# Performance work log

Measured on AMD Instinct MI355X. Metric: run time of the kernel, lower is better.

The kernel has to match this reference:

```python
import jax, jax.numpy as jnp
import numpy as np


def setup_inputs() -> dict:
    key = jax.random.key(0)
    k1, k2, k3, k4, k5 = jax.random.split(key, 5)
    B, T, H = 8, 2048, 1024
    s = 1.0 / np.sqrt(H)
    return {
        "x": jax.random.normal(k1, (B, T, H), dtype=jnp.float32),
        "W_ih": jax.random.normal(k2, (3 * H, H), dtype=jnp.float32) * s,
        "b_ih": jax.random.normal(k3, (3 * H,), dtype=jnp.float32) * s,
        "W_hh": jax.random.normal(k4, (3 * H, H), dtype=jnp.float32) * s,
        "b_hh": jax.random.normal(k5, (3 * H,), dtype=jnp.float32) * s,
    }


def reference(x, W_ih, b_ih, W_hh, b_hh):
    # x: [B, T, H]; W_ih/W_hh: [3H, H]; biases: [3H]
    B, T, H = x.shape
    # Precompute input-to-hidden projection in one batched matmul: [B, T, 3H]
    x_proj = jnp.einsum("bth,gh->btg", x, W_ih) + b_ih
    h0 = jnp.zeros((B, H), dtype=x.dtype)

    def step(h, g_x):
        # g_x: [B, 3H]
        g_h = h @ W_hh.T + b_hh  # [B, 3H]
        r = jax.nn.sigmoid(g_x[:, :H] + g_h[:, :H])
        z = jax.nn.sigmoid(g_x[:, H:2 * H] + g_h[:, H:2 * H])
        n = jnp.tanh(g_x[:, 2 * H:] + r * g_h[:, 2 * H:])
        h_new = (1 - z) * n + z * h
        return h_new, h_new

    # scan over time axis: move T to leading axis
    _, out = jax.lax.scan(step, h0, jnp.swapaxes(x_proj, 0, 1))  # out: [T, B, H]
    return jnp.swapaxes(out, 0, 1)  # [B, T, H]; dropout=0.0 (eval) is identity
```

## Files before the change

kernel.cpp:

```cpp
#include <hip/hip_runtime.h>

#define T_STEPS 2048
#define BATCH 8
#define HID 1024

#define XPROJ_F 50331648ull
#define HBUF64_BYTE_OFF 201326592ull

__device__ __forceinline__ float sigmoidf_(float x) {
    return 1.0f / (1.0f + __expf(-x));
}

__device__ __forceinline__ unsigned long long ld_u64_agent(const unsigned long long* p) {
    return __hip_atomic_load(p, __ATOMIC_RELAXED, __HIP_MEMORY_SCOPE_AGENT);
}
__device__ __forceinline__ void st_u64_agent(unsigned long long* p, unsigned long long v) {
    __hip_atomic_store(p, v, __ATOMIC_RELAXED, __HIP_MEMORY_SCOPE_AGENT);
}

__global__ __launch_bounds__(256) void gemm_xproj(
        const float* __restrict__ x, const float* __restrict__ Wih,
        const float* __restrict__ bih, float* __restrict__ xproj) {
    __shared__ float a_lds[16][128];
    __shared__ float b_lds[16][128];
    const int tid = threadIdx.x;
    const int m0 = blockIdx.x * 128;
    const int n0 = blockIdx.y * 128;
    const int tx = tid & 15, ty = tid >> 4;

    float acc[8][8];
#pragma unroll
    for (int i = 0; i < 8; i++)
#pragma unroll
        for (int jj = 0; jj < 8; jj++) acc[i][jj] = 0.f;

    for (int k0 = 0; k0 < 1024; k0 += 16) {
#pragma unroll
        for (int l = 0; l < 2; l++) {
            const int c = tid + l * 256;
            const int row = c >> 2;
            const int f4 = c & 3;
            float4 av = *reinterpret_cast<const float4*>(
                x + (size_t)(m0 + row) * 1024 + k0 + f4 * 4);
            float4 bv = *reinterpret_cast<const float4*>(
                Wih + (size_t)(n0 + row) * 1024 + k0 + f4 * 4);
            a_lds[f4 * 4 + 0][row] = av.x; a_lds[f4 * 4 + 1][row] = av.y;
            a_lds[f4 * 4 + 2][row] = av.z; a_lds[f4 * 4 + 3][row] = av.w;
            b_lds[f4 * 4 + 0][row] = bv.x; b_lds[f4 * 4 + 1][row] = bv.y;
            b_lds[f4 * 4 + 2][row] = bv.z; b_lds[f4 * 4 + 3][row] = bv.w;
        }
        __syncthreads();
#pragma unroll
        for (int kk = 0; kk < 16; kk++) {
            float a[8], b[8];
            *reinterpret_cast<float4*>(&a[0]) =
                *reinterpret_cast<float4*>(&a_lds[kk][ty * 8]);
            *reinterpret_cast<float4*>(&a[4]) =
                *reinterpret_cast<float4*>(&a_lds[kk][ty * 8 + 4]);
            *reinterpret_cast<float4*>(&b[0]) =
                *reinterpret_cast<float4*>(&b_lds[kk][tx * 8]);
            *reinterpret_cast<float4*>(&b[4]) =
                *reinterpret_cast<float4*>(&b_lds[kk][tx * 8 + 4]);
#pragma unroll
            for (int i = 0; i < 8; i++)
#pragma unroll
                for (int jj = 0; jj < 8; jj++)
                    acc[i][jj] = fmaf(a[i], b[jj], acc[i][jj]);
        }
        __syncthreads();
    }

    float bias[8];
    *reinterpret_cast<float4*>(&bias[0]) =
        *reinterpret_cast<const float4*>(bih + n0 + tx * 8);
    *reinterpret_cast<float4*>(&bias[4]) =
        *reinterpret_cast<const float4*>(bih + n0 + tx * 8 + 4);
    const int n_base = n0 + tx * 8;
    const int g = n_base >> 10;
    const int j0 = n_base & 1023;
#pragma unroll
    for (int i = 0; i < 8; i++) {
        const int m = m0 + ty * 8 + i;
        const int b = m >> 11;
        const int t = m & 2047;
        float* dst = xproj + (((size_t)t * 8 + b) * 3 + g) * 1024 + j0;
        float4 r0 = {acc[i][0] + bias[0], acc[i][1] + bias[1],
                     acc[i][2] + bias[2], acc[i][3] + bias[3]};
        float4 r1 = {acc[i][4] + bias[4], acc[i][5] + bias[5],
                     acc[i][6] + bias[6], acc[i][7] + bias[7]};
        *reinterpret_cast<float4*>(dst) = r0;
        *reinterpret_cast<float4*>(dst + 4) = r1;
    }
}

__global__ __launch_bounds__(256, 1) void gru_scan(
        const float* __restrict__ Whh, const float* __restrict__ bhh,
        const float* __restrict__ xproj, float* __restrict__ out,
        unsigned long long* __restrict__ hbuf64) {
    __shared__ float hshare[2][2 * HID];
    const int tid = threadIdx.x;
    const int bid = blockIdx.x;
    const int wave = tid >> 6;
    const int lane = tid & 63;
    const int group = bid >> 6;
    const int gb = bid & 63;
    const int b0 = group * 2;
    const int jbase = gb * 16 + wave * 4;

    float wf[3][4][16];
#pragma unroll
    for (int g = 0; g < 3; g++)
#pragma unroll
        for (int jj = 0; jj < 4; jj++)
#pragma unroll
            for (int i = 0; i < 16; i++)
                wf[g][jj][i] =
                    Whh[(size_t)(g * 1024 + jbase + jj) * 1024 + lane + 64 * i];

    const int jj_l = lane >> 1;
    const int bb_l = lane & 1;
    const int j_l = jbase + jj_l;
    const int b_l = b0 + bb_l;
    float bh0 = 0.f, bh1 = 0.f, bh2 = 0.f;
    if (lane < 8) {
        bh0 = bhh[j_l];
        bh1 = bhh[1024 + j_l];
        bh2 = bhh[2048 + j_l];
    }

    if (lane < 8) {
        const size_t xb = ((size_t)0 * 8 + b_l) * 3 * 1024 + j_l;
        const float gxr = xproj[xb];
        const float gxz = xproj[xb + 1024];
        const float gxn = xproj[xb + 2048];
        const float r = sigmoidf_(gxr + bh0);
        const float z = sigmoidf_(gxz + bh1);
        const float n = tanhf(gxn + r * bh2);
        const float hnew = (1.f - z) * n;
        st_u64_agent(hbuf64 + (size_t)b_l * HID + j_l,
                     ((unsigned long long)1u << 32) | __float_as_uint(hnew));
        out[(size_t)b_l * T_STEPS * HID + j_l] = hnew;
    }

    for (int t = 1; t < T_STEPS; t++) {
        float gxr = 0.f, gxz = 0.f, gxn = 0.f;
        if (lane < 8) {
            const size_t xb = ((size_t)t * 8 + b_l) * 3 * 1024 + j_l;
            gxr = xproj[xb];
            gxz = xproj[xb + 1024];
            gxn = xproj[xb + 2048];
        }

        const int par = (t - 1) & 1;
        const unsigned long long* src =
            hbuf64 + (size_t)par * 8192 + (size_t)b0 * HID;
        const unsigned expect = (unsigned)t;
        unsigned long long v[8];
#pragma unroll
        for (int i = 0; i < 8; i++)
            v[i] = ld_u64_agent(src + tid + 256 * i);
        for (;;) {
            unsigned bad = 0;
#pragma unroll
            for (int i = 0; i < 8; i++)
                bad |= (unsigned)(v[i] >> 32) ^ expect;
            if (bad == 0) break;
            __builtin_amdgcn_s_sleep(1);
#pragma unroll
            for (int i = 0; i < 8; i++)
                if ((unsigned)(v[i] >> 32) != expect)
                    v[i] = ld_u64_agent(src + tid + 256 * i);
        }
#pragma unroll
        for (int i = 0; i < 8; i++)
            hshare[par][tid + 256 * i] = __uint_as_float((unsigned)v[i]);
        __syncthreads();

        const float hprev = (lane < 8) ? hshare[par][bb_l * HID + j_l] : 0.f;

        float acc[3][8];
#pragma unroll
        for (int g = 0; g < 3; g++)
#pragma unroll
            for (int q = 0; q < 8; q++) acc[g][q] = 0.f;
#pragma unroll
        for (int bb = 0; bb < 2; bb++) {
            float hv[16];
#pragma unroll
            for (int i = 0; i < 16; i++)
                hv[i] = hshare[par][bb * HID + lane + 64 * i];
#pragma unroll
            for (int g = 0; g < 3; g++)
#pragma unroll
                for (int jj = 0; jj < 4; jj++)
#pragma unroll
                    for (int i = 0; i < 16; i++)
                        acc[g][jj * 2 + bb] =
                            fmaf(wf[g][jj][i], hv[i], acc[g][jj * 2 + bb]);
        }

        float a4[3][4];
#pragma unroll
        for (int g = 0; g < 3; g++)
#pragma unroll
            for (int k = 0; k < 4; k++) {
                const float e = acc[g][2 * k], o = acc[g][2 * k + 1];
                const float give = (lane & 1) ? e : o;
                const float keep = (lane & 1) ? o : e;
                a4[g][k] = keep + __shfl_xor(give, 1);
            }
        float a2[3][2];
#pragma unroll
        for (int g = 0; g < 3; g++)
#pragma unroll
            for (int k = 0; k < 2; k++) {
                const float e = a4[g][2 * k], o = a4[g][2 * k + 1];
                const float give = (lane & 2) ? e : o;
                const float keep = (lane & 2) ? o : e;
                a2[g][k] = keep + __shfl_xor(give, 2);
            }
        float a1[3];
#pragma unroll
        for (int g = 0; g < 3; g++) {
            const float e = a2[g][0], o = a2[g][1];
            const float give = (lane & 4) ? e : o;
            const float keep = (lane & 4) ? o : e;
            a1[g] = keep + __shfl_xor(give, 4);
        }
#pragma unroll
        for (int m = 8; m <= 32; m <<= 1)
#pragma unroll
            for (int g = 0; g < 3; g++) a1[g] += __shfl_xor(a1[g], m);

        if (lane < 8) {
            const float r = sigmoidf_(gxr + a1[0] + bh0);
            const float z = sigmoidf_(gxz + a1[1] + bh1);
            const float n = tanhf(gxn + r * (a1[2] + bh2));
            const float hnew = (1.f - z) * n + z * hprev;
            st_u64_agent(hbuf64 + (size_t)(t & 1) * 8192 + (size_t)b_l * HID + j_l,
                         ((unsigned long long)(unsigned)(t + 1) << 32) |
                             __float_as_uint(hnew));
            out[((size_t)b_l * T_STEPS + t) * HID + j_l] = hnew;
        }
    }
}

extern "C" void kernel_launch(void* const* d_in, const int* in_sizes, int n_in,
                              void* d_out, int out_size, void* d_ws,
                              size_t ws_size, hipStream_t stream) {
    const float* x    = (const float*)d_in[0];
    const float* Wih  = (const float*)d_in[1];
    const float* bih  = (const float*)d_in[2];
    const float* Whh  = (const float*)d_in[3];
    const float* bhh  = (const float*)d_in[4];
    float* outp = (float*)d_out;

    float* xproj = (float*)d_ws;
    unsigned long long* hbuf64 =
        (unsigned long long*)((char*)d_ws + HBUF64_BYTE_OFF);

    dim3 g1(128, 24);
    gemm_xproj<<<g1, 256, 0, stream>>>(x, Wih, bih, xproj);
    gru_scan<<<256, 256, 0, stream>>>(Whh, bhh, xproj, outp, hbuf64);
}
```

Measured before the change: 8.267 ms.

## Pack two hidden values per flag word and assign one batch per block

Each block now handles one batch row and 32 hidden units instead of two batch rows and 16, so it holds twice the W_hh slice in registers. Hidden-state exchange packs two floats into each 64-bit word and uses bit 30 of the low float as a parity tag instead of a full 32-bit step counter. Hidden values are clamped just below 1 so that bit is always free. This halves the polled global traffic per block and reduces spin-wait loads. The cost is more register pressure, with a risk of spills, and the xproj layout is switched to batch-major to match.

```diff
diff --git a/kernel.cpp b/kernel.cpp
--- a/kernel.cpp
+++ b/kernel.cpp
@@ -83,7 +83,7 @@
         const int m = m0 + ty * 8 + i;
         const int b = m >> 11;
         const int t = m & 2047;
-        float* dst = xproj + (((size_t)t * 8 + b) * 3 + g) * 1024 + j0;
+        float* dst = xproj + (((size_t)b * 2048 + t) * 3 + g) * 1024 + j0;
         float4 r0 = {acc[i][0] + bias[0], acc[i][1] + bias[1],
                      acc[i][2] + bias[2], acc[i][3] + bias[3]};
         float4 r1 = {acc[i][4] + bias[4], acc[i][5] + bias[5],
@@ -97,106 +97,102 @@
         const float* __restrict__ Whh, const float* __restrict__ bhh,
         const float* __restrict__ xproj, float* __restrict__ out,
         unsigned long long* __restrict__ hbuf64) {
-    __shared__ float hshare[2][2 * HID];
+    __shared__ float hshare[2][HID];
     const int tid = threadIdx.x;
     const int bid = blockIdx.x;
     const int wave = tid >> 6;
     const int lane = tid & 63;
-    const int group = bid >> 6;
-    const int gb = bid & 63;
-    const int b0 = group * 2;
-    const int jbase = gb * 16 + wave * 4;
-
-    float wf[3][4][16];
+    const int b = bid & 7;
+    const int gb = bid >> 3;
+    const int jb_w = gb * 32 + wave * 8;
+    const int jw = jb_w + (lane & 7);
+
+    float wf[3][8][16];
 #pragma unroll
     for (int g = 0; g < 3; g++)
 #pragma unroll
-        for (int jj = 0; jj < 4; jj++)
+        for (int jj = 0; jj < 8; jj++)
 #pragma unroll
             for (int i = 0; i < 16; i++)
                 wf[g][jj][i] =
-                    Whh[(size_t)(g * 1024 + jbase + jj) * 1024 + lane + 64 * i];
-
-    const int jj_l = lane >> 1;
-    const int bb_l = lane & 1;
-    const int j_l = jbase + jj_l;
-    const int b_l = b0 + bb_l;
-    float bh0 = 0.f, bh1 = 0.f, bh2 = 0.f;
-    if (lane < 8) {
-        bh0 = bhh[j_l];
-        bh1 = bhh[1024 + j_l];
-        bh2 = bhh[2048 + j_l];
-    }
-
-    if (lane < 8) {
-        const size_t xb = ((size_t)0 * 8 + b_l) * 3 * 1024 + j_l;
+                    Whh[(size_t)(g * 1024 + jb_w + jj) * 1024 + lane + 64 * i];
+
+    const float bh0 = bhh[jw];
+    const float bh1 = bhh[1024 + jw];
+    const float bh2 = bhh[2048 + jw];
+    const float CL = 0x1.fffffep-1f;
+
+    {
+        const size_t xb = ((size_t)b * 2048 + 0) * 3 * 1024 + jw;
         const float gxr = xproj[xb];
         const float gxz = xproj[xb + 1024];
         const float gxn = xproj[xb + 2048];
         const float r = sigmoidf_(gxr + bh0);
         const float z = sigmoidf_(gxz + bh1);
         const float n = tanhf(gxn + r * bh2);
-        const float hnew = (1.f - z) * n;
-        st_u64_agent(hbuf64 + (size_t)b_l * HID + j_l,
-                     ((unsigned long long)1u << 32) | __float_as_uint(hnew));
-        out[(size_t)b_l * T_STEPS * HID + j_l] = hnew;
+        float hnew = (1.f - z) * n;
+        hnew = fminf(fmaxf(hnew, -CL), CL);
+        const float hodd = __shfl_xor(hnew, 1);
+        const unsigned lo = __float_as_uint(hnew) | (1u << 30);
+        const unsigned hi = __float_as_uint(hodd);
+        if (lane < 8) {
+            if ((lane & 1) == 0)
+                st_u64_agent(hbuf64 + (size_t)b * 512 + ((jb_w + lane) >> 1),
+                             ((unsigned long long)hi << 32) | lo);
+            out[((size_t)b * 2048 + 0) * 1024 + jw] = hnew;
+        }
     }
 
     for (int t = 1; t < T_STEPS; t++) {
-        float gxr = 0.f, gxz = 0.f, gxn = 0.f;
-        if (lane < 8) {
-            const size_t xb = ((size_t)t * 8 + b_l) * 3 * 1024 + j_l;
-            gxr = xproj[xb];
-            gxz = xproj[xb + 1024];
-            gxn = xproj[xb + 2048];
-        }
+        const size_t xb = ((size_t)b * 2048 + t) * 3 * 1024 + jw;
+        const float gxr = xproj[xb];
+        const float gxz = xproj[xb + 1024];
+        const float gxn = xproj[xb + 2048];
 
         const int par = (t - 1) & 1;
         const unsigned long long* src =
-            hbuf64 + (size_t)par * 8192 + (size_t)b0 * HID;
-        const unsigned expect = (unsigned)t;
-        unsigned long long v[8];
-#pragma unroll
-        for (int i = 0; i < 8; i++)
-            v[i] = ld_u64_agent(src + tid + 256 * i);
+            hbuf64 + (size_t)par * 4096 + (size_t)b * 512;
+        const unsigned expect = (((unsigned)(t - 1) >> 1) & 1u) ^ 1u;
+        unsigned long long v0 = ld_u64_agent(src + tid);
+        unsigned long long v1 = ld_u64_agent(src + tid + 256);
         for (;;) {
-            unsigned bad = 0;
-#pragma unroll
-            for (int i = 0; i < 8; i++)
-                bad |= (unsigned)(v[i] >> 32) ^ expect;
-            if (bad == 0) break;
+            const unsigned t0 = ((unsigned)(v0 >> 30)) & 1u;
+            const unsigned t1 = ((unsigned)(v1 >> 30)) & 1u;
+            if (((t0 ^ expect) | (t1 ^ expect)) == 0u) break;
             __builtin_amdgcn_s_sleep(1);
-#pragma unroll
-            for (int i = 0; i < 8; i++)
-                if ((unsigned)(v[i] >> 32) != expect)
-                    v[i] = ld_u64_agent(src + tid + 256 * i);
-        }
-#pragma unroll
-        for (int i = 0; i < 8; i++)
-            hshare[par][tid + 256 * i] = __uint_as_float((unsigned)v[i]);
+            if (t0 != expect) v0 = ld_u64_agent(src + tid);
+            if (t1 != expect) v1 = ld_u64_agent(src + tid + 256);
+        }
+        {
+            float2 p0, p1;
+            p0.x = __uint_as_float((unsigned)v0 & 0xBFFFFFFFu);
+            p0.y = __uint_as_float((unsigned)(v0 >> 32));
+            p1.x = __uint_as_float((unsigned)v1 & 0xBFFFFFFFu);
+            p1.y = __uint_as_float((unsigned)(v1 >> 32));
+            *reinterpret_cast<float2*>(&hshare[par][2 * tid]) = p0;
+            *reinterpret_cast<float2*>(&hshare[par][2 * tid + 512]) = p1;
+        }
         __syncthreads();
 
-        const float hprev = (lane < 8) ? hshare[par][bb_l * HID + j_l] : 0.f;
+        const float hprev = hshare[par][jw];
 
         float acc[3][8];
 #pragma unroll
         for (int g = 0; g < 3; g++)
 #pragma unroll
             for (int q = 0; q < 8; q++) acc[g][q] = 0.f;
-#pragma unroll
-        for (int bb = 0; bb < 2; bb++) {
+        {
             float hv[16];
 #pragma unroll
             for (int i = 0; i < 16; i++)
-                hv[i] = hshare[par][bb * HID + lane + 64 * i];
+                hv[i] = hshare[par][lane + 64 * i];
 #pragma unroll
             for (int g = 0; g < 3; g++)
 #pragma unroll
-                for (int jj = 0; jj < 4; jj++)
+                for (int jj = 0; jj < 8; jj++)
 #pragma unroll
                     for (int i = 0; i < 16; i++)
-                        acc[g][jj * 2 + bb] =
-                            fmaf(wf[g][jj][i], hv[i], acc[g][jj * 2 + bb]);
+                        acc[g][jj] = fmaf(wf[g][jj][i], hv[i], acc[g][jj]);
         }
 
         float a4[3][4];
@@ -232,15 +228,21 @@
 #pragma unroll
             for (int g = 0; g < 3; g++) a1[g] += __shfl_xor(a1[g], m);
 
+        const float r = sigmoidf_(gxr + a1[0] + bh0);
+        const float z = sigmoidf_(gxz + a1[1] + bh1);
+        const float n = tanhf(gxn + r * (a1[2] + bh2));
+        float hnew = (1.f - z) * n + z * hprev;
+        hnew = fminf(fmaxf(hnew, -CL), CL);
+        const float hodd = __shfl_xor(hnew, 1);
+        const unsigned tagst = (((unsigned)t >> 1) & 1u) ^ 1u;
+        const unsigned lo = __float_as_uint(hnew) | (tagst << 30);
+        const unsigned hi = __float_as_uint(hodd);
         if (lane < 8) {
-            const float r = sigmoidf_(gxr + a1[0] + bh0);
-            const float z = sigmoidf_(gxz + a1[1] + bh1);
-            const float n = tanhf(gxn + r * (a1[2] + bh2));
-            const float hnew = (1.f - z) * n + z * hprev;
-            st_u64_agent(hbuf64 + (size_t)(t & 1) * 8192 + (size_t)b_l * HID + j_l,
-                         ((unsigned long long)(unsigned)(t + 1) << 32) |
-                             __float_as_uint(hnew));
-            out[((size_t)b_l * T_STEPS + t) * HID + j_l] = hnew;
+            if ((lane & 1) == 0)
+                st_u64_agent(hbuf64 + (size_t)(t & 1) * 4096 + (size_t)b * 512 +
+                                 ((jb_w + lane) >> 1),
+                             ((unsigned long long)hi << 32) | lo);
+            out[((size_t)b * 2048 + t) * 1024 + jw] = hnew;
         }
     }
 }
```

Result: slower. 9.999 ms (+20.9%).
